# Optimization experiments

Hardware: AMD Instinct MI355X
Metric: run time of the kernel (lower is better)

The kernel has to match this reference:

```python
import jax, jax.numpy as jnp
import numpy as np

N_NODES, N_EDGES, BATCH = 50000, 100000, 256
H = 64            # dim_hidden_features
D_NODE, D_EDGE, D_RBF = 110, 8, 8
D_SET = 2 * H     # Set2Set input_dim = 128, output_dim = 256
D_HID = 512
D_CAT = 54
MP_STEPS, S2S_ITERS = 4, 3


def setup_inputs() -> dict:
    key = jax.random.key(0)
    ks = iter(jax.random.split(key, 48))

    def nrm(shape, s=0.05):
        return jax.random.normal(next(ks), shape, dtype=jnp.float32) * s

    inp = {}
    inp["node_attribute"] = jax.random.normal(next(ks), (N_NODES, D_NODE), dtype=jnp.float32)
    inp["edge_attribute"] = jax.random.normal(next(ks), (N_EDGES, D_EDGE), dtype=jnp.float32)
    inp["edge_length"] = jax.random.uniform(next(ks), (N_EDGES,), dtype=jnp.float32)
    inp["src"] = jax.random.randint(next(ks), (N_EDGES,), 0, N_NODES, dtype=jnp.int32)
    inp["dst"] = jax.random.randint(next(ks), (N_EDGES,), 0, N_NODES, dtype=jnp.int32)
    inp["node_graph"] = jnp.sort(jax.random.randint(next(ks), (N_NODES,), 0, BATCH, dtype=jnp.int32))
    # atom_feature_projector
    inp["proj_W"] = nrm((D_NODE, H)); inp["proj_b"] = jnp.zeros((H,), jnp.float32)
    # RBF layer: centers ~ U(0,1), beta = 10 (per reset_parameters)
    inp["centers"] = jax.random.uniform(next(ks), (D_RBF,), dtype=jnp.float32)
    inp["beta"] = jnp.full((D_RBF,), 10.0, jnp.float32)
    # NNConv edge function: Linear(16 -> 64*64), plus NNConv bias
    inp["bond_W"] = nrm((D_EDGE + D_RBF, H * H)); inp["bond_b"] = jnp.zeros((H * H,), jnp.float32)
    inp["conv_b"] = jnp.zeros((H,), jnp.float32)
    # GRU (input H, hidden H); PyTorch layout (3H, in)
    inp["gru_Wih"] = nrm((3 * H, H)); inp["gru_Whh"] = nrm((3 * H, H))
    inp["gru_bih"] = jnp.zeros((3 * H,), jnp.float32); inp["gru_bhh"] = jnp.zeros((3 * H,), jnp.float32)
    # Set2Set LSTM: input 2*D_SET=256, hidden D_SET=128, 2 layers; PyTorch layout (4H, in)
    inp["lstm_Wih0"] = nrm((4 * D_SET, 2 * D_SET)); inp["lstm_Whh0"] = nrm((4 * D_SET, D_SET))
    inp["lstm_bih0"] = jnp.zeros((4 * D_SET,), jnp.float32); inp["lstm_bhh0"] = jnp.zeros((4 * D_SET,), jnp.float32)
    inp["lstm_Wih1"] = nrm((4 * D_SET, D_SET)); inp["lstm_Whh1"] = nrm((4 * D_SET, D_SET))
    inp["lstm_bih1"] = jnp.zeros((4 * D_SET,), jnp.float32); inp["lstm_bhh1"] = jnp.zeros((4 * D_SET,), jnp.float32)
    # sparsify: Linear(256 -> 512) + PReLU(init 0.25)
    inp["sp_W"] = nrm((2 * D_SET, D_HID)); inp["sp_b"] = jnp.zeros((D_HID,), jnp.float32)
    inp["prelu_a"] = jnp.array([0.25], jnp.float32)
    # catalyst1 head: hiddens[0] (512->512 ReLU, 512->512 Tanh) then outputs[0] (512->54)
    inp["h0_W1"] = nrm((D_HID, D_HID)); inp["h0_b1"] = jnp.zeros((D_HID,), jnp.float32)
    inp["h0_W2"] = nrm((D_HID, D_HID)); inp["h0_b2"] = jnp.zeros((D_HID,), jnp.float32)
    inp["out_W"] = nrm((D_HID, D_CAT)); inp["out_b"] = jnp.zeros((D_CAT,), jnp.float32)
    return inp


def _lstm_cell(x, h, c, Wih, Whh, bih, bhh):
    # PyTorch LSTM gate order: i, f, g, o
    g = x @ Wih.T + bih + h @ Whh.T + bhh
    i, f, gg, o = jnp.split(g, 4, axis=-1)
    c = jax.nn.sigmoid(f) * c + jax.nn.sigmoid(i) * jnp.tanh(gg)
    h = jax.nn.sigmoid(o) * jnp.tanh(c)
    return h, c


def reference(node_attribute, edge_attribute, edge_length, src, dst, node_graph,
              proj_W, proj_b, centers, beta, bond_W, bond_b, conv_b,
              gru_Wih, gru_Whh, gru_bih, gru_bhh,
              lstm_Wih0, lstm_Whh0, lstm_bih0, lstm_bhh0,
              lstm_Wih1, lstm_Whh1, lstm_bih1, lstm_bhh1,
              sp_W, sp_b, prelu_a, h0_W1, h0_b1, h0_W2, h0_b2, out_W, out_b):
    n_nodes = node_attribute.shape[0]
    # atom feature projection
    x = jax.nn.relu(node_attribute @ proj_W + proj_b)                       # (N, H)
    # edge features = [edge_attribute, RBF(length)]
    rbf = jnp.exp(-beta * (edge_length[:, None] - centers[None, :]) ** 2)   # (E, 8)
    efeat = jnp.concatenate([edge_attribute, rbf], axis=-1)                 # (E, 16)
    # NNConv per-edge weight matrix; edge features are constant over MP steps
    W_e = (efeat @ bond_W + bond_b).reshape(-1, H, H)                       # (E, H, H)

    feat, h = x, x
    for _ in range(MP_STEPS):
        # NNConv: message = h_src @ W_e, sum-aggregated at dst, plus bias
        m = jnp.einsum('ei,eio->eo', feat[src], W_e)                        # (E, H)
        agg = jax.ops.segment_sum(m, dst, num_segments=n_nodes) + conv_b    # (N, H)
        gx = jax.nn.relu(agg)
        # GRU cell (PyTorch gate order r, z, n)
        gi = gx @ gru_Wih.T + gru_bih
        gh = h @ gru_Whh.T + gru_bhh
        i_r, i_z, i_n = jnp.split(gi, 3, axis=-1)
        h_r, h_z, h_n = jnp.split(gh, 3, axis=-1)
        r = jax.nn.sigmoid(i_r + h_r)
        z = jax.nn.sigmoid(i_z + h_z)
        n = jnp.tanh(i_n + r * h_n)
        h = (1.0 - z) * n + z * h
        feat = h
    node_agg = jnp.concatenate([feat, x], axis=-1)                          # (N, 2H)

    # Set2Set pooling over graphs (segment softmax attention, 2-layer LSTM)
    B = BATCH
    h0 = c0 = jnp.zeros((B, D_SET), node_agg.dtype)
    h1 = c1 = jnp.zeros((B, D_SET), node_agg.dtype)
    q_star = jnp.zeros((B, 2 * D_SET), node_agg.dtype)
    for _ in range(S2S_ITERS):
        h0, c0 = _lstm_cell(q_star, h0, c0, lstm_Wih0, lstm_Whh0, lstm_bih0, lstm_bhh0)
        h1, c1 = _lstm_cell(h0, h1, c1, lstm_Wih1, lstm_Whh1, lstm_bih1, lstm_bhh1)
        q = h1                                                              # (B, 128)
        e = jnp.sum(node_agg * q[node_graph], axis=-1)                      # (N,)
        emax = jax.ops.segment_max(e, node_graph, num_segments=B)
        p = jnp.exp(e - emax[node_graph])
        denom = jax.ops.segment_sum(p, node_graph, num_segments=B)
        alpha = p / denom[node_graph]                                       # per-graph softmax
        r_out = jax.ops.segment_sum(node_agg * alpha[:, None], node_graph, num_segments=B)
        q_star = jnp.concatenate([q, r_out], axis=-1)                       # (B, 256)

    # sparsify (Linear + PReLU)
    feats = q_star @ sp_W + sp_b                                            # (B, 512)
    feats = jnp.where(feats >= 0, feats, prelu_a * feats)
    # catalyst1 head
    hid = jnp.tanh(jax.nn.relu(feats @ h0_W1 + h0_b1) @ h0_W2 + h0_b2)
    return jax.nn.softmax(hid @ out_W + out_b, axis=-1)                     # (B, 54)
```

## Files before the change

kernel.cpp:

```cpp
#include <hip/hip_runtime.h>
#include <math.h>

constexpr int N = 50000;
constexpr int E = 100000;
constexpr int B = 256;
constexpr int H = 64;
constexpr int DN = 110;
constexpr int NBLK = (E + 63) / 64;

#define DEV __device__ __forceinline__

typedef __attribute__((ext_vector_type(8))) short short8;
typedef __attribute__((ext_vector_type(4))) float floatx4;

DEV float sigf(float x) { return 1.0f / (1.0f + expf(-x)); }

DEV short f2bf(float f) {
    unsigned u = __float_as_uint(f);
    unsigned r = (u + 0x7fffu + ((u >> 16) & 1u)) >> 16;
    return (short)r;
}
DEV float bf2f(short s) { return __uint_as_float(((unsigned)(unsigned short)s) << 16); }

DEV void cvt8(const float* p, short8& hi, short8& lo) {
    float4 u0 = *(const float4*)p;
    float4 u1 = *(const float4*)(p + 4);
    float vv[8] = {u0.x, u0.y, u0.z, u0.w, u1.x, u1.y, u1.z, u1.w};
#pragma unroll
    for (int j = 0; j < 8; ++j) {
        short hb = f2bf(vv[j]);
        hi[j] = hb;
        lo[j] = f2bf(vv[j] - bf2f(hb));
    }
}

__global__ void k_izero(int* p, int n) {
    int i = blockIdx.x * 256 + threadIdx.x;
    if (i < n) p[i] = 0;
}

DEV void d_transpose(const float* in, float* out, int R, int C, int idx) {
    int r = idx / C, c = idx % C;
    out[c * R + r] = in[idx];
}

DEV void d_prepB(const float* __restrict__ W, short* __restrict__ out,
                 int NT16, int ld, int trans, int ocap, int kcap, int idx) {
    int lane = idx & 63;
    int t = idx >> 6;
    int ntile = t % NT16;
    int kt = t / NT16;
    int quad = lane >> 4, col = lane & 15;
    int o = ntile * 16 + col;
    short hi[8], lo[8];
#pragma unroll
    for (int j = 0; j < 8; ++j) {
        int k = kt * 32 + quad * 8 + j;
        float v = 0.0f;
        if (o < ocap && k < kcap) v = trans ? W[(size_t)o * ld + k] : W[(size_t)k * ld + o];
        short hb = f2bf(v);
        hi[j] = hb;
        lo[j] = f2bf(v - bf2f(hb));
    }
    short* dh = out + (((size_t)(t * 2 + 0) * 64 + lane) * 8);
    short* dl = out + (((size_t)(t * 2 + 1) * 64 + lane) * 8);
#pragma unroll
    for (int j = 0; j < 8; ++j) { dh[j] = hi[j]; dl[j] = lo[j]; }
}

DEV void d_prepW(const float* __restrict__ bond_W, const float* __restrict__ bond_b,
                 short* __restrict__ wf, int idx) {
    int lane = idx & 63;
    int t = idx >> 6;
    int ks = t & 1;
    int nt = (t >> 1) & 3;
    int kk = t >> 3;
    const float* S = (kk < 16) ? (bond_W + kk * 4096) : bond_b;
    int quad = lane >> 4, col = lane & 15;
    short hi[8], lo[8];
#pragma unroll
    for (int j = 0; j < 8; ++j) {
        int i = ks * 32 + quad * 8 + j;
        float v = S[i * 64 + nt * 16 + col];
        short hb = f2bf(v);
        hi[j] = hb;
        lo[j] = f2bf(v - bf2f(hb));
    }
    short* dh = wf + (((size_t)(t * 2 + 0) * 64 + lane) * 8);
    short* dl = wf + (((size_t)(t * 2 + 1) * 64 + lane) * 8);
#pragma unroll
    for (int j = 0; j < 8; ++j) { dh[j] = hi[j]; dl[j] = lo[j]; }
}

__launch_bounds__(256)
__global__ void k_prep0(const float* lWih0, const float* lWhh0, const float* lWih1, const float* lWhh1,
                        float* lW0T, float* lU0T, float* lW1T, float* lU1T,
                        const float* bond_W, const float* bond_b, short* wf,
                        const float* gru_Wih, const float* gru_Whh, short* fgI, short* fgH,
                        const float* proj_W, short* fproj,
                        float* zreg) {
    int idx = blockIdx.x * 256 + threadIdx.x;
    if (idx < 131072) { d_transpose(lWih0, lW0T, 512, 256, idx); return; }
    idx -= 131072;
    if (idx < 65536) { d_transpose(lWhh0, lU0T, 512, 128, idx); return; }
    idx -= 65536;
    if (idx < 65536) { d_transpose(lWih1, lW1T, 512, 128, idx); return; }
    idx -= 65536;
    if (idx < 65536) { d_transpose(lWhh1, lU1T, 512, 128, idx); return; }
    idx -= 65536;
    if (idx < 8704) { d_prepW(bond_W, bond_b, wf, idx); return; }
    idx -= 8704;
    if (idx < 1536) { d_prepB(gru_Wih, fgI, 12, 64, 1, 192, 64, idx); return; }
    idx -= 1536;
    if (idx < 1536) { d_prepB(gru_Whh, fgH, 12, 64, 1, 192, 64, idx); return; }
    idx -= 1536;
    if (idx < 1024) { d_prepB(proj_W, fproj, 4, 64, 0, 64, DN, idx); return; }
    idx -= 1024;
    if (idx < 196608) { zreg[idx] = 0.0f; return; }
}
constexpr int PREP0_TOTAL = 131072 + 3 * 65536 + 8704 + 2 * 1536 + 1024 + 196608;

__launch_bounds__(256)
__global__ void k_prephead(const float* sp_W, short* fsp, const float* h0_W1, short* fw1,
                           const float* h0_W2, short* fw2, const float* out_W, short* fow) {
    int idx = blockIdx.x * 256 + threadIdx.x;
    if (idx < 16384) { d_prepB(sp_W, fsp, 32, 512, 0, 512, 256, idx); return; }
    idx -= 16384;
    if (idx < 32768) { d_prepB(h0_W1, fw1, 32, 512, 0, 512, 512, idx); return; }
    idx -= 32768;
    if (idx < 32768) { d_prepB(h0_W2, fw2, 32, 512, 0, 512, 512, idx); return; }
    idx -= 32768;
    if (idx < 4096) { d_prepB(out_W, fow, 4, 54, 0, 54, 512, idx); return; }
}
constexpr int PREPH_TOTAL = 16384 + 2 * 32768 + 4096;

__global__ void k_deg(const int* __restrict__ dst, int* __restrict__ deg) {
    int e = blockIdx.x * 256 + threadIdx.x;
    if (e < E) atomicAdd(&deg[dst[e]], 1);
}
__global__ void k_scan1(const int* __restrict__ deg, int* __restrict__ bsum) {
    __shared__ int s[256];
    int b = blockIdx.x, tid = threadIdx.x;
    int idx = b * 256 + tid;
    s[tid] = (idx < N) ? deg[idx] : 0;
    __syncthreads();
    for (int st = 128; st > 0; st >>= 1) {
        if (tid < st) s[tid] += s[tid + st];
        __syncthreads();
    }
    if (tid == 0) bsum[b] = s[0];
}
__global__ void k_scan2p(int* __restrict__ bsum, int nb) {
    __shared__ int s[256];
    int tid = threadIdx.x;
    int v = (tid < nb) ? bsum[tid] : 0;
    s[tid] = v;
    __syncthreads();
    for (int off = 1; off < 256; off <<= 1) {
        int t = (tid >= off) ? s[tid - off] : 0;
        __syncthreads();
        s[tid] += t;
        __syncthreads();
    }
    if (tid < nb) bsum[tid] = s[tid] - v;
}
__global__ void k_scan3(const int* __restrict__ deg, const int* __restrict__ bsum,
                        int* __restrict__ cursor, int* __restrict__ roff) {
    __shared__ int s[256];
    int b = blockIdx.x, tid = threadIdx.x;
    int idx = b * 256 + tid;
    int v = (idx < N) ? deg[idx] : 0;
    s[tid] = v;
    __syncthreads();
    for (int off = 1; off < 256; off <<= 1) {
        int t = (tid >= off) ? s[tid - off] : 0;
        __syncthreads();
        s[tid] += t;
        __syncthreads();
    }
    if (idx < N) {
        int start = bsum[b] + s[tid] - v;
        cursor[idx] = start;
        roff[idx] = start;
    }
    if (idx == 0) roff[N] = E;
}
__global__ void k_scat(const int* __restrict__ src, const int* __restrict__ dst,
                       int* __restrict__ cursor, int* __restrict__ srcp,
                       int* __restrict__ epos, int* __restrict__ dstp) {
    int e = blockIdx.x * 256 + threadIdx.x;
    if (e >= E) return;
    int d = dst[e];
    int pos = atomicAdd(&cursor[d], 1);
    srcp[pos] = src[e];
    dstp[pos] = d;
    epos[e] = pos;
}

__launch_bounds__(256)
__global__ void k_projm(const float* __restrict__ na, const short* __restrict__ fp,
                        const float* __restrict__ b, float* __restrict__ x,
                        short* __restrict__ hs) {
    __shared__ float as[16 * 132];
    int tid = threadIdx.x, lane = tid & 63, nt = tid >> 6;
    int quad = lane >> 4, col = lane & 15;
    int s0 = blockIdx.x * 16;
    for (int i = tid; i < 16 * DN; i += 256) {
        int r = i / DN, c = i % DN;
        as[r * 132 + c] = na[(size_t)s0 * DN + i];
    }
    for (int i = tid; i < 16 * 22; i += 256) {
        int r = i / 22, c = DN + i % 22;
        as[r * 132 + c] = 0.0f;
    }
    __syncthreads();
    const short8* F = (const short8*)fp;
    floatx4 T = {0.0f, 0.0f, 0.0f, 0.0f};
#pragma unroll
    for (int kt = 0; kt < 4; ++kt) {
        const float* ap = as + col * 132 + kt * 32 + quad * 8;
        short8 ah, al;
#pragma unroll
        for (int j = 0; j < 8; ++j) {
            float v = ap[j];
            short hb = f2bf(v);
            ah[j] = hb;
            al[j] = f2bf(v - bf2f(hb));
        }
        int t = kt * 4 + nt;
        short8 bh = F[(t * 2 + 0) * 64 + lane];
        short8 bl = F[(t * 2 + 1) * 64 + lane];
        T = __builtin_amdgcn_mfma_f32_16x16x32_bf16(ah, bh, T, 0, 0, 0);
        T = __builtin_amdgcn_mfma_f32_16x16x32_bf16(al, bh, T, 0, 0, 0);
        T = __builtin_amdgcn_mfma_f32_16x16x32_bf16(ah, bl, T, 0, 0, 0);
    }
    int o = nt * 16 + col;
    float bo = b[o];
#pragma unroll
    for (int r = 0; r < 4; ++r) {
        int n = s0 + quad * 4 + r;
        float v = fmaxf(T[r] + bo, 0.0f);
        x[(size_t)n * 64 + o] = v;
        short hb = f2bf(v);
        hs[(size_t)n * 128 + o] = hb;
        hs[(size_t)n * 128 + 64 + o] = f2bf(v - bf2f(hb));
    }
}

__global__ void k_efeat2(const float* __restrict__ ea, const float* __restrict__ el,
                         const float* __restrict__ centers, const float* __restrict__ beta,
                         const int* __restrict__ epos, float* __restrict__ ef_t) {
    int e = blockIdx.x * 256 + threadIdx.x;
    if (e >= E) return;
    int pos = epos[e];
    float L = el[e];
#pragma unroll
    for (int j = 0; j < 8; ++j) ef_t[j * E + pos] = ea[e * 8 + j];
#pragma unroll
    for (int j = 0; j < 8; ++j) {
        float d = L - centers[j];
        ef_t[(8 + j) * E + pos] = expf(-beta[j] * d * d);
    }
    ef_t[16 * E + pos] = 1.0f;
}

__launch_bounds__(256)
__global__ void k_msgagg(const short* __restrict__ hs, const float* __restrict__ ef_t,
                         const short* __restrict__ wf, const int* __restrict__ srcp,
                         const int* __restrict__ dstp,
                         float* __restrict__ agg, float* __restrict__ bpart) {
    __shared__ float efs[17 * 64];
    __shared__ int srcs[64];
    __shared__ int dsh[64];
    __shared__ int shprev;
    __shared__ float Csh[64][68];
    __shared__ float psum[4][64], ssum[4][64];
    __shared__ int pd[4], sd[4], whole[4];

    int tid = threadIdx.x;
    int e0 = blockIdx.x * 64;
    int lane = tid & 63;
    int nt = tid >> 6;
    int quad = lane >> 4, col = lane & 15;

    if (tid < 64) {
        int eg = e0 + tid;
        srcs[tid] = (eg < E) ? srcp[eg] : 0;
        dsh[tid] = (eg < E) ? dstp[eg] : N;
    }
    if (tid == 0) shprev = (e0 == 0) ? -1 : dstp[e0 - 1];
    for (int i = tid; i < 17 * 64; i += 256) {
        int kk = i >> 6, e = i & 63;
        int eg = e0 + e;
        efs[i] = (eg < E) ? ef_t[(size_t)kk * E + eg] : 0.0f;
    }
    __syncthreads();

    short8 Ah[4][2], Al[4][2];
#pragma unroll
    for (int mt = 0; mt < 4; ++mt) {
        int s = srcs[mt * 16 + col];
        const short* hp = hs + (size_t)s * 128 + quad * 8;
#pragma unroll
        for (int ks = 0; ks < 2; ++ks) {
            Ah[mt][ks] = *(const short8*)(hp + ks * 32);
            Al[mt][ks] = *(const short8*)(hp + 64 + ks * 32);
        }
    }

    const short8* Wf = (const short8*)wf;
    float C[4][4] = {};

#define LOADB(d0, d1, d2, d3, KK)                      \
    {                                                  \
        int tb_ = ((KK) * 4 + nt) * 2;                 \
        d0 = Wf[((tb_ + 0) * 2 + 0) * 64 + lane];      \
        d1 = Wf[((tb_ + 1) * 2 + 0) * 64 + lane];      \
        d2 = Wf[((tb_ + 0) * 2 + 1) * 64 + lane];      \
        d3 = Wf[((tb_ + 1) * 2 + 1) * 64 + lane];      \
    }

    short8 c0, c1, c2, c3, n0_, n1_, n2_, n3_, q0, q1, q2, q3;
    LOADB(c0, c1, c2, c3, 0);
    LOADB(n0_, n1_, n2_, n3_, 1);
    LOADB(q0, q1, q2, q3, 2);

#pragma unroll 1
    for (int kk = 0; kk < 17; ++kk) {
        int kn = kk + 3;
        if (kn > 16) kn = 16;
        short8 p0, p1, p2, p3;
        LOADB(p0, p1, p2, p3, kn);

#pragma unroll
        for (int mt = 0; mt < 4; ++mt) {
            floatx4 T = {0.0f, 0.0f, 0.0f, 0.0f};
            T = __builtin_amdgcn_mfma_f32_16x16x32_bf16(Ah[mt][0], c0, T, 0, 0, 0);
            T = __builtin_amdgcn_mfma_f32_16x16x32_bf16(Ah[mt][1], c1, T, 0, 0, 0);
            T = __builtin_amdgcn_mfma_f32_16x16x32_bf16(Al[mt][0], c0, T, 0, 0, 0);
            T = __builtin_amdgcn_mfma_f32_16x16x32_bf16(Al[mt][1], c1, T, 0, 0, 0);
            T = __builtin_amdgcn_mfma_f32_16x16x32_bf16(Ah[mt][0], c2, T, 0, 0, 0);
            T = __builtin_amdgcn_mfma_f32_16x16x32_bf16(Ah[mt][1], c3, T, 0, 0, 0);
            float4 ef = *(const float4*)&efs[kk * 64 + mt * 16 + quad * 4];
            C[mt][0] += ef.x * T[0];
            C[mt][1] += ef.y * T[1];
            C[mt][2] += ef.z * T[2];
            C[mt][3] += ef.w * T[3];
        }
        c0 = n0_; c1 = n1_; c2 = n2_; c3 = n3_;
        n0_ = q0; n1_ = q1; n2_ = q2; n3_ = q3;
        q0 = p0; q1 = p1; q2 = p2; q3 = p3;
    }
#undef LOADB

#pragma unroll
    for (int mt = 0; mt < 4; ++mt)
#pragma unroll
        for (int r = 0; r < 4; ++r)
            Csh[mt * 16 + quad * 4 + r][nt * 16 + col] = C[mt][r];
    __syncthreads();

    {
        int c = lane;
        int base = nt * 16;
        int prevd = (nt == 0) ? shprev : dsh[base - 1];
        int cur = dsh[base];
        int gcap = cur < N ? cur : N;
        for (int q = prevd + 1; q < gcap; ++q) agg[(size_t)q * 64 + c] = 0.0f;
        if (cur >= N) {
            if (lane == 0) { pd[nt] = -2; sd[nt] = -2; whole[nt] = 0; }
        } else {
            float acc = 0.0f;
            int ntr = 0;
            bool done = false;
            for (int r = base; r < base + 16; ++r) {
                int d = dsh[r];
                if (d != cur) {
                    if (ntr == 0) {
                        psum[nt][c] = acc;
                        if (lane == 0) pd[nt] = cur;
                    } else {
                        agg[(size_t)cur * 64 + c] = acc;
                    }
                    ++ntr;
                    int dc = d < N ? d : N;
                    for (int q = cur + 1; q < dc; ++q) agg[(size_t)q * 64 + c] = 0.0f;
                    cur = d; acc = 0.0f;
                    if (cur >= N) { done = true; break; }
                }
                acc += Csh[r][c];
            }
            if (!done) {
                if (ntr == 0) {
                    psum[nt][c] = acc;
                    if (lane == 0) { pd[nt] = cur; sd[nt] = cur; whole[nt] = 1; }
                } else {
                    ssum[nt][c] = acc;
                    if (lane == 0) { sd[nt] = cur; whole[nt] = 0; }
                }
            } else {
                if (lane == 0) { sd[nt] = -2; whole[nt] = 0; }
            }
        }
    }
    __syncthreads();

    if (tid < 64) {
        int c = tid;
        int cur = -1;
        float acc = 0.0f;
        bool ownedCur = false;
        bool first = true;
        int firstd = dsh[0];
#pragma unroll
        for (int w = 0; w < 4; ++w) {
            int p = pd[w];
            if (p < 0) continue;
            float s = psum[w][c];
            if (first) {
                cur = p; acc = s;
                ownedCur = (e0 == 0) || (firstd != shprev);
                first = false;
            } else if (p == cur) {
                acc += s;
            } else {
                if (ownedCur) agg[(size_t)cur * 64 + c] = acc;
                else bpart[(size_t)blockIdx.x * 64 + c] = acc;
                cur = p; acc = s; ownedCur = true;
            }
            if (!whole[w] && sd[w] >= 0) {
                int sdd = sd[w];
                float s2 = ssum[w][c];
                if (sdd == cur) {
                    acc += s2;
                } else {
                    if (ownedCur) agg[(size_t)cur * 64 + c] = acc;
                    else bpart[(size_t)blockIdx.x * 64 + c] = acc;
                    cur = sdd; acc = s2; ownedCur = true;
                }
            }
        }
        if (!first) {
            if (ownedCur) agg[(size_t)cur * 64 + c] = acc;
            else bpart[(size_t)blockIdx.x * 64 + c] = acc;
        }
    }
}

__launch_bounds__(256)
__global__ void k_gru4(const float* __restrict__ agg, const float* __restrict__ bpart,
                       const int* __restrict__ roff, const float* __restrict__ conv_b,
                       short* __restrict__ hs,
                       const short* __restrict__ fI, const short* __restrict__ fH,
                       const float* __restrict__ bih, const float* __restrict__ bhh) {
    int tid = threadIdx.x, lane = tid & 63, nt = tid >> 6;
    int quad = lane >> 4, col = lane & 15;
    int n0 = blockIdx.x * 32;

    short8 Gh[2][2], Gl[2][2], Hh[2][2], Hl[2][2];
#pragma unroll
    for (int mt = 0; mt < 2; ++mt) {
        int node = n0 + mt * 16 + col;
        bool ok = node < N;
        int nc = ok ? node : (N - 1);
        float acc[2][8];
        const float* ag = agg + (size_t)nc * 64;
#pragma unroll
        for (int ks = 0; ks < 2; ++ks) {
            const float* cb = conv_b + ks * 32 + quad * 8;
            float4 a0 = *(const float4*)(ag + ks * 32 + quad * 8);
            float4 a1 = *(const float4*)(ag + ks * 32 + quad * 8 + 4);
            acc[ks][0] = a0.x + cb[0]; acc[ks][1] = a0.y + cb[1];
            acc[ks][2] = a0.z + cb[2]; acc[ks][3] = a0.w + cb[3];
            acc[ks][4] = a1.x + cb[4]; acc[ks][5] = a1.y + cb[5];
            acc[ks][6] = a1.z + cb[6]; acc[ks][7] = a1.w + cb[7];
        }
        int rs = roff[nc];
        int re = roff[nc + 1];
        if (re > rs) {
            int b0 = rs >> 6, b1 = (re - 1) >> 6;
            for (int bb = b0 + 1; bb <= b1; ++bb) {
                const float* bp = bpart + (size_t)bb * 64;
#pragma unroll
                for (int ks = 0; ks < 2; ++ks) {
                    float4 p0 = *(const float4*)(bp + ks * 32 + quad * 8);
                    float4 p1 = *(const float4*)(bp + ks * 32 + quad * 8 + 4);
                    acc[ks][0] += p0.x; acc[ks][1] += p0.y;
                    acc[ks][2] += p0.z; acc[ks][3] += p0.w;
                    acc[ks][4] += p1.x; acc[ks][5] += p1.y;
                    acc[ks][6] += p1.z; acc[ks][7] += p1.w;
                }
            }
        }
        const short* hp = hs + (size_t)nc * 128 + quad * 8;
#pragma unroll
        for (int ks = 0; ks < 2; ++ks) {
            short8 hh8 = *(const short8*)(hp + ks * 32);
            short8 hl8 = *(const short8*)(hp + 64 + ks * 32);
            Hh[mt][ks] = hh8;
            Hl[mt][ks] = hl8;
#pragma unroll
            for (int j = 0; j < 8; ++j) {
                float g = ok ? fmaxf(acc[ks][j], 0.0f) : 0.0f;
                short gb = f2bf(g);
                Gh[mt][ks][j] = gb;
                Gl[mt][ks][j] = f2bf(g - bf2f(gb));
            }
        }
        if (!ok) {
#pragma unroll
            for (int ks = 0; ks < 2; ++ks) {
                Hh[mt][ks] = short8{0,0,0,0,0,0,0,0};
                Hl[mt][ks] = short8{0,0,0,0,0,0,0,0};
            }
        }
    }
    __syncthreads();

    const short8* FI = (const short8*)fI;
    const short8* FH = (const short8*)fH;
    floatx4 aI[2][3] = {}, aH[2][3] = {};
#pragma unroll
    for (int ks = 0; ks < 2; ++ks) {
        short8 bIh[3], bIl[3], bHh[3], bHl[3];
#pragma unroll
        for (int g = 0; g < 3; ++g) {
            int t = ks * 12 + g * 4 + nt;
            bIh[g] = FI[(t * 2 + 0) * 64 + lane];
            bIl[g] = FI[(t * 2 + 1) * 64 + lane];
            bHh[g] = FH[(t * 2 + 0) * 64 + lane];
            bHl[g] = FH[(t * 2 + 1) * 64 + lane];
        }
#pragma unroll
        for (int mt = 0; mt < 2; ++mt) {
#pragma unroll
            for (int g = 0; g < 3; ++g) {
                aI[mt][g] = __builtin_amdgcn_mfma_f32_16x16x32_bf16(Gh[mt][ks], bIh[g], aI[mt][g], 0, 0, 0);
                aI[mt][g] = __builtin_amdgcn_mfma_f32_16x16x32_bf16(Gl[mt][ks], bIh[g], aI[mt][g], 0, 0, 0);
                aI[mt][g] = __builtin_amdgcn_mfma_f32_16x16x32_bf16(Gh[mt][ks], bIl[g], aI[mt][g], 0, 0, 0);
                aH[mt][g] = __builtin_amdgcn_mfma_f32_16x16x32_bf16(Hh[mt][ks], bHh[g], aH[mt][g], 0, 0, 0);
                aH[mt][g] = __builtin_amdgcn_mfma_f32_16x16x32_bf16(Hl[mt][ks], bHh[g], aH[mt][g], 0, 0, 0);
                aH[mt][g] = __builtin_amdgcn_mfma_f32_16x16x32_bf16(Hh[mt][ks], bHl[g], aH[mt][g], 0, 0, 0);
            }
        }
    }

    int o = nt * 16 + col;
    float br = bih[o], bz = bih[64 + o], bn = bih[128 + o];
    float cr = bhh[o], cz = bhh[64 + o], cn = bhh[128 + o];
#pragma unroll
    for (int mt = 0; mt < 2; ++mt) {
#pragma unroll
        for (int r = 0; r < 4; ++r) {
            int node = n0 + mt * 16 + quad * 4 + r;
            if (node >= N) continue;
            float rg = sigf(aI[mt][0][r] + br + aH[mt][0][r] + cr);
            float z  = sigf(aI[mt][1][r] + bz + aH[mt][1][r] + cz);
            float ng = tanhf(aI[mt][2][r] + bn + rg * (aH[mt][2][r] + cn));
            size_t hb_ = (size_t)node * 128 + o;
            float hold = bf2f(hs[hb_]) + bf2f(hs[hb_ + 64]);
            float hn = (1.0f - z) * ng + z * hold;
            short hi = f2bf(hn);
            hs[hb_] = hi;
            hs[hb_ + 64] = f2bf(hn - bf2f(hi));
        }
    }
}

__global__ void k_bounds2(const int* __restrict__ ng, int* __restrict__ gs, int* __restrict__ ge) {
    int n = blockIdx.x * 256 + threadIdx.x;
    if (n >= N) return;
    int g = ng[n];
    int gp = (n == 0) ? -1 : ng[n - 1];
    if (g != gp) {
        gs[g] = n;
        if (n > 0) ge[gp] = n;
        for (int q = gp + 1; q < g; ++q) { gs[q] = 0; ge[q] = 0; }
    }
    if (n == N - 1) {
        ge[g] = N;
        for (int q = g + 1; q < B; ++q) { gs[q] = 0; ge[q] = 0; }
    }
}

__launch_bounds__(256)
__global__ void k_s2s(float* __restrict__ h0, float* __restrict__ c0,
                      float* __restrict__ h1, float* __restrict__ c1,
                      float* __restrict__ q_star,
                      const float* __restrict__ W0T, const float* __restrict__ U0T,
                      const float* __restrict__ b0i, const float* __restrict__ b0h,
                      const float* __restrict__ W1T, const float* __restrict__ U1T,
                      const float* __restrict__ b1i, const float* __restrict__ b1h,
                      const short* __restrict__ hs, const float* __restrict__ x,
                      const int* __restrict__ gs, const int* __restrict__ ge) {
    __shared__ float xb[256], hb[128], gb[512], h0n[128], qv[128];
    __shared__ float mrg[4][2][64];
    __shared__ float ml[4][2];
    int g = blockIdx.x, tid = threadIdx.x;
    xb[tid] = q_star[g * 256 + tid];
    if (tid < 128) hb[tid] = h0[g * 128 + tid];
    __syncthreads();
    float g0 = b0i[tid] + b0h[tid];
    float g1 = b0i[tid + 256] + b0h[tid + 256];
    for (int i = 0; i < 256; ++i) {
        float xx = xb[i];
        g0 += xx * W0T[i * 512 + tid];
        g1 += xx * W0T[i * 512 + tid + 256];
    }
    for (int i = 0; i < 128; ++i) {
        float hh = hb[i];
        g0 += hh * U0T[i * 512 + tid];
        g1 += hh * U0T[i * 512 + tid + 256];
    }
    gb[tid] = g0; gb[tid + 256] = g1;
    __syncthreads();
    if (tid < 128) {
        float ii = gb[tid], ff = gb[128 + tid], gg = gb[256 + tid], oo = gb[384 + tid];
        float c = sigf(ff) * c0[g * 128 + tid] + sigf(ii) * tanhf(gg);
        float hn = sigf(oo) * tanhf(c);
        c0[g * 128 + tid] = c; h0[g * 128 + tid] = hn; h0n[tid] = hn;
        hb[tid] = h1[g * 128 + tid];
    }
    __syncthreads();
    float ga = b1i[tid] + b1h[tid];
    float gbv = b1i[tid + 256] + b1h[tid + 256];
    for (int i = 0; i < 128; ++i) {
        float xx = h0n[i], hh = hb[i];
        ga  += xx * W1T[i * 512 + tid]       + hh * U1T[i * 512 + tid];
        gbv += xx * W1T[i * 512 + tid + 256] + hh * U1T[i * 512 + tid + 256];
    }
    gb[tid] = ga; gb[tid + 256] = gbv;
    __syncthreads();
    if (tid < 128) {
        float ii = gb[tid], ff = gb[128 + tid], gg = gb[256 + tid], oo = gb[384 + tid];
        float c = sigf(ff) * c1[g * 128 + tid] + sigf(ii) * tanhf(gg);
        float hn = sigf(oo) * tanhf(c);
        c1[g * 128 + tid] = c; h1[g * 128 + tid] = hn;
        q_star[g * 256 + tid] = hn;
        qv[tid] = hn;
    }
    __syncthreads();
    int s0v = gs[g], s1v = ge[g];
    int lane = tid & 63, grp = tid >> 6;
    float qh = qv[lane], qx = qv[64 + lane];
    float mM = -INFINITY, lL = 0.0f, nh = 0.0f, nx = 0.0f;
    for (int n = s0v + grp; n < s1v; n += 16) {
        float hv[4], xv[4], e[4];
#pragma unroll
        for (int j = 0; j < 4; ++j) {
            int nj = n + 4 * j;
            int nc = (nj < s1v) ? nj : n;
            hv[j] = bf2f(hs[(size_t)nc * 128 + lane]) + bf2f(hs[(size_t)nc * 128 + 64 + lane]);
            xv[j] = x[(size_t)nc * 64 + lane];
            e[j] = hv[j] * qh + xv[j] * qx;
        }
#pragma unroll
        for (int off = 32; off; off >>= 1) {
#pragma unroll
            for (int j = 0; j < 4; ++j) e[j] += __shfl_xor(e[j], off, 64);
        }
#pragma unroll
        for (int j = 0; j < 4; ++j)
            if (n + 4 * j >= s1v) e[j] = -INFINITY;
        float mb = fmaxf(fmaxf(e[0], e[1]), fmaxf(e[2], e[3]));
        float mn = fmaxf(mM, mb);
        float sc = expf(mM - mn);
        float w0 = expf(e[0] - mn), w1 = expf(e[1] - mn);
        float w2 = expf(e[2] - mn), w3 = expf(e[3] - mn);
        lL = lL * sc + ((w0 + w1) + (w2 + w3));
        nh = nh * sc + ((w0 * hv[0] + w1 * hv[1]) + (w2 * hv[2] + w3 * hv[3]));
        nx = nx * sc + ((w0 * xv[0] + w1 * xv[1]) + (w2 * xv[2] + w3 * xv[3]));
        mM = mn;
    }
    mrg[grp][0][lane] = nh;
    mrg[grp][1][lane] = nx;
    if (lane == 0) { ml[grp][0] = mM; ml[grp][1] = lL; }
    __syncthreads();
    if (tid < 128) {
        int half = tid >> 6, dl = tid & 63;
        float M = -INFINITY;
#pragma unroll
        for (int i = 0; i < 4; ++i) M = fmaxf(M, ml[i][0]);
        float L = 0.0f, NUM = 0.0f;
#pragma unroll
        for (int i = 0; i < 4; ++i) {
            float sc = expf(ml[i][0] - M);
            L += ml[i][1] * sc;
            NUM += mrg[i][half][dl] * sc;
        }
        q_star[g * 256 + 128 + tid] = (s1v > s0v) ? NUM / L : 0.0f;
    }
}

template<int MODE>
__launch_bounds__(256)
__global__ void k_hgemm(const float* __restrict__ A, const short* __restrict__ Bf,
                        const float* __restrict__ bias, const float* __restrict__ pa,
                        float* __restrict__ Cout, int K, int NT16) {
    int tid = threadIdx.x, lane = tid & 63, nt = tid >> 6;
    int quad = lane >> 4, col = lane & 15;
    int s0 = blockIdx.x * 16;
    int ntile = blockIdx.y * 4 + nt;
    int NoutTot = NT16 * 16;
    const short8* F = (const short8*)Bf;
    floatx4 T = {0.0f, 0.0f, 0.0f, 0.0f};
    const float* ap = A + (size_t)(s0 + col) * K + quad * 8;
    int KT = K >> 5;
#pragma unroll 4
    for (int kt = 0; kt < KT; ++kt) {
        short8 ah, al;
        cvt8(ap + kt * 32, ah, al);
        int t = kt * NT16 + ntile;
        short8 bh = F[(t * 2 + 0) * 64 + lane];
        short8 bl = F[(t * 2 + 1) * 64 + lane];
        T = __builtin_amdgcn_mfma_f32_16x16x32_bf16(ah, bh, T, 0, 0, 0);
        T = __builtin_amdgcn_mfma_f32_16x16x32_bf16(al, bh, T, 0, 0, 0);
        T = __builtin_amdgcn_mfma_f32_16x16x32_bf16(ah, bl, T, 0, 0, 0);
    }
    int o = ntile * 16 + col;
    float b = bias[o];
    float a = (MODE == 0) ? pa[0] : 0.0f;
#pragma unroll
    for (int r = 0; r < 4; ++r) {
        float v = T[r] + b;
        if (MODE == 0) v = (v >= 0.0f) ? v : a * v;
        if (MODE == 1) v = fmaxf(v, 0.0f);
        if (MODE == 2) v = tanhf(v);
        Cout[(size_t)(s0 + quad * 4 + r) * NoutTot + o] = v;
    }
}

__launch_bounds__(256)
__global__ void k_hout(const float* __restrict__ A, const short* __restrict__ Bf,
                       const float* __restrict__ ob, float* __restrict__ out) {
    __shared__ float sm[16][64];
    __shared__ float smax[16], sinv[16];
    int tid = threadIdx.x, lane = tid & 63, nt = tid >> 6;
    int quad = lane >> 4, col = lane & 15;
    int s0 = blockIdx.x * 16;
    const short8* F = (const short8*)Bf;
    floatx4 T = {0.0f, 0.0f, 0.0f, 0.0f};
    const float* ap = A + (size_t)(s0 + col) * 512 + quad * 8;
#pragma unroll 4
    for (int kt = 0; kt < 16; ++kt) {
        short8 ah, al;
        cvt8(ap + kt * 32, ah, al);
        int t = kt * 4 + nt;
        short8 bh = F[(t * 2 + 0) * 64 + lane];
        short8 bl = F[(t * 2 + 1) * 64 + lane];
        T = __builtin_amdgcn_mfma_f32_16x16x32_bf16(ah, bh, T, 0, 0, 0);
        T = __builtin_amdgcn_mfma_f32_16x16x32_bf16(al, bh, T, 0, 0, 0);
        T = __builtin_amdgcn_mfma_f32_16x16x32_bf16(ah, bl, T, 0, 0, 0);
    }
    int o = nt * 16 + col;
    float b = (o < 54) ? ob[o] : 0.0f;
#pragma unroll
    for (int r = 0; r < 4; ++r)
        sm[quad * 4 + r][o] = (o < 54) ? (T[r] + b) : -1e30f;
    __syncthreads();
    if (tid < 16) {
        float m = -INFINITY;
        for (int j = 0; j < 54; ++j) m = fmaxf(m, sm[tid][j]);
        float s = 0.0f;
        for (int j = 0; j < 54; ++j) s += expf(sm[tid][j] - m);
        smax[tid] = m;
        sinv[tid] = 1.0f / s;
    }
    __syncthreads();
    for (int idx = tid; idx < 16 * 54; idx += 256) {
        int srow = idx / 54, oo = idx % 54;
        out[(size_t)(s0 + srow) * 54 + oo] = expf(sm[srow][oo] - smax[srow]) * sinv[srow];
    }
}

extern "C" void kernel_launch(void* const* d_in, const int* in_sizes, int n_in,
                              void* d_out, int out_size, void* d_ws, size_t ws_size,
                              hipStream_t stream) {
    const float* node_attr = (const float*)d_in[0];
    const float* edge_attr = (const float*)d_in[1];
    const float* edge_len  = (const float*)d_in[2];
    const int*   src       = (const int*)d_in[3];
    const int*   dst       = (const int*)d_in[4];
    const int*   node_grph = (const int*)d_in[5];
    const float* proj_W    = (const float*)d_in[6];
    const float* proj_b    = (const float*)d_in[7];
    const float* centers   = (const float*)d_in[8];
    const float* beta      = (const float*)d_in[9];
    const float* bond_W    = (const float*)d_in[10];
    const float* bond_b    = (const float*)d_in[11];
    const float* conv_b    = (const float*)d_in[12];
    const float* gru_Wih   = (const float*)d_in[13];
    const float* gru_Whh   = (const float*)d_in[14];
    const float* gru_bih   = (const float*)d_in[15];
    const float* gru_bhh   = (const float*)d_in[16];
    const float* lWih0     = (const float*)d_in[17];
    const float* lWhh0     = (const float*)d_in[18];
    const float* lbih0     = (const float*)d_in[19];
    const float* lbhh0     = (const float*)d_in[20];
    const float* lWih1     = (const float*)d_in[21];
    const float* lWhh1     = (const float*)d_in[22];
    const float* lbih1     = (const float*)d_in[23];
    const float* lbhh1     = (const float*)d_in[24];
    const float* sp_W      = (const float*)d_in[25];
    const float* sp_b      = (const float*)d_in[26];
    const float* prelu_a   = (const float*)d_in[27];
    const float* h0_W1     = (const float*)d_in[28];
    const float* h0_b1     = (const float*)d_in[29];
    const float* h0_W2     = (const float*)d_in[30];
    const float* h0_b2     = (const float*)d_in[31];
    const float* out_W     = (const float*)d_in[32];
    const float* out_b     = (const float*)d_in[33];
    float* out = (float*)d_out;

    float* ws = (float*)d_ws;
    size_t off = 0;
    float* x      = ws + off; off += (size_t)N * 64;
    float* hsf    = ws + off; off += (size_t)N * 64;
    float* ef_t   = ws + off; off += (size_t)E * 17;
    float* agg    = ws + off; off += (size_t)N * 64;
    float* wfrag  = ws + off; off += 17 * 16 * 64 * 8 / 2;
    float* fgI    = ws + off; off += 2 * 64 * 192 / 2;
    float* fgH    = ws + off; off += 2 * 64 * 192 / 2;
    float* fproj  = ws + off; off += 16 * 1024 / 2;
    float* lW0T   = ws + off; off += 256 * 512;
    float* lU0T   = ws + off; off += 128 * 512;
    float* lW1T   = ws + off; off += 128 * 512;
    float* lU1T   = ws + off; off += 128 * 512;
    float* h0     = ws + off; off += B * 128;
    float* c0     = ws + off; off += B * 128;
    float* h1     = ws + off; off += B * 128;
    float* c1     = ws + off; off += B * 128;
    float* q_star = ws + off; off += B * 256;
    float* bpart  = ws + off; off += (size_t)NBLK * 64;
    int* gs       = (int*)(ws + off); off += B;
    int* ge       = (int*)(ws + off); off += B;
    int* deg      = (int*)(ws + off); off += N;
    int* cursor   = (int*)(ws + off); off += N;
    int* roff     = (int*)(ws + off); off += N + 1;
    int* bsum     = (int*)(ws + off); off += 256;
    int* srcp     = (int*)(ws + off); off += E;
    int* epos     = (int*)(ws + off); off += E;
    int* dstp     = (int*)(ws + off); off += E;

    short* hs = (short*)hsf;

    short* fsp = (short*)ef_t;
    short* fw1 = (short*)(ef_t + 131072);
    short* fw2 = (short*)(ef_t + 131072 + 262144);
    short* fow = (short*)(ef_t + 131072 + 2 * 262144);
    float* hb1 = ef_t + 131072 + 2 * 262144 + 32768;
    float* hb2 = hb1 + 131072;

    constexpr int NB = (N + 255) / 256;

    k_izero<<<NB, 256, 0, stream>>>(deg, N);
    k_deg<<<(E + 255) / 256, 256, 0, stream>>>(dst, deg);
    k_scan1<<<NB, 256, 0, stream>>>(deg, bsum);
    k_scan2p<<<1, 256, 0, stream>>>(bsum, NB);
    k_scan3<<<NB, 256, 0, stream>>>(deg, bsum, cursor, roff);
    k_scat<<<(E + 255) / 256, 256, 0, stream>>>(src, dst, cursor, srcp, epos, dstp);

    k_prep0<<<(PREP0_TOTAL + 255) / 256, 256, 0, stream>>>(
        lWih0, lWhh0, lWih1, lWhh1, lW0T, lU0T, lW1T, lU1T,
        bond_W, bond_b, (short*)wfrag, gru_Wih, gru_Whh, (short*)fgI, (short*)fgH,
        proj_W, (short*)fproj, h0);

    k_projm<<<N / 16, 256, 0, stream>>>(node_attr, (const short*)fproj, proj_b, x, hs);
    k_efeat2<<<(E + 255) / 256, 256, 0, stream>>>(edge_attr, edge_len, centers, beta, epos, ef_t);

    k_bounds2<<<(N + 255) / 256, 256, 0, stream>>>(node_grph, gs, ge);

    for (int step = 0; step < 4; ++step) {
        k_msgagg<<<NBLK, 256, 0, stream>>>(hs, ef_t, (const short*)wfrag, srcp, dstp,
                                           agg, bpart);
        k_gru4<<<(N + 31) / 32, 256, 0, stream>>>(agg, bpart, roff, conv_b, hs,
                                                  (const short*)fgI, (const short*)fgH,
                                                  gru_bih, gru_bhh);
    }

    k_prephead<<<(PREPH_TOTAL + 255) / 256, 256, 0, stream>>>(
        sp_W, fsp, h0_W1, fw1, h0_W2, fw2, out_W, fow);

    for (int it = 0; it < 3; ++it) {
        k_s2s<<<B, 256, 0, stream>>>(h0, c0, h1, c1, q_star,
                                     lW0T, lU0T, lbih0, lbhh0,
                                     lW1T, lU1T, lbih1, lbhh1,
                                     hs, x, gs, ge);
    }

    k_hgemm<0><<<dim3(16, 8), 256, 0, stream>>>(q_star, fsp, sp_b, prelu_a, hb1, 256, 32);
    k_hgemm<1><<<dim3(16, 8), 256, 0, stream>>>(hb1, fw1, h0_b1, nullptr, hb2, 512, 32);
    k_hgemm<2><<<dim3(16, 8), 256, 0, stream>>>(hb2, fw2, h0_b2, nullptr, hb1, 512, 32);
    k_hout<<<16, 256, 0, stream>>>(hb1, fow, out_b, out);
}
```

Measured before the change: 733.4 us.

## Process 128 edges per block in NNConv message kernel to reuse edge weights

Doubles the edges handled per block in the fused message/aggregate kernel from 64 to 128. Each wave now holds eight 16-edge A tiles, so every loaded slice of the edge-network weights feeds twice as many MFMAs. Source-feature gathers are issued straight from global memory ahead of the shared-memory staging to overlap latency. The weight prefetch depth drops from three stages to two to make room in registers. The trade-off is higher register and LDS use, hence lower occupancy, plus half as many blocks and longer serial segment scans.

```diff
diff --git a/kernel.cpp b/kernel.cpp
--- a/kernel.cpp
+++ b/kernel.cpp
@@ -6,7 +6,8 @@
 constexpr int B = 256;
 constexpr int H = 64;
 constexpr int DN = 110;
-constexpr int NBLK = (E + 63) / 64;
+constexpr int EPB = 128;
+constexpr int NBLK = (E + EPB - 1) / EPB;
 
 #define DEV __device__ __forceinline__
 
@@ -269,37 +270,24 @@
                          const short* __restrict__ wf, const int* __restrict__ srcp,
                          const int* __restrict__ dstp,
                          float* __restrict__ agg, float* __restrict__ bpart) {
-    __shared__ float efs[17 * 64];
-    __shared__ int srcs[64];
-    __shared__ int dsh[64];
+    __shared__ float efs[17 * EPB];
+    __shared__ int dsh[EPB];
     __shared__ int shprev;
-    __shared__ float Csh[64][68];
+    __shared__ float Csh[EPB][68];
     __shared__ float psum[4][64], ssum[4][64];
     __shared__ int pd[4], sd[4], whole[4];
 
     int tid = threadIdx.x;
-    int e0 = blockIdx.x * 64;
+    int e0 = blockIdx.x * EPB;
     int lane = tid & 63;
     int nt = tid >> 6;
     int quad = lane >> 4, col = lane & 15;
 
-    if (tid < 64) {
-        int eg = e0 + tid;
-        srcs[tid] = (eg < E) ? srcp[eg] : 0;
-        dsh[tid] = (eg < E) ? dstp[eg] : N;
-    }
-    if (tid == 0) shprev = (e0 == 0) ? -1 : dstp[e0 - 1];
-    for (int i = tid; i < 17 * 64; i += 256) {
-        int kk = i >> 6, e = i & 63;
-        int eg = e0 + e;
-        efs[i] = (eg < E) ? ef_t[(size_t)kk * E + eg] : 0.0f;
-    }
-    __syncthreads();
-
-    short8 Ah[4][2], Al[4][2];
-#pragma unroll
-    for (int mt = 0; mt < 4; ++mt) {
-        int s = srcs[mt * 16 + col];
+    short8 Ah[8][2], Al[8][2];
+#pragma unroll
+    for (int mt = 0; mt < 8; ++mt) {
+        int eg = e0 + mt * 16 + col;
+        int s = (eg < E) ? srcp[eg] : 0;
         const short* hp = hs + (size_t)s * 128 + quad * 8;
 #pragma unroll
         for (int ks = 0; ks < 2; ++ks) {
@@ -308,8 +296,20 @@
         }
     }
 
+    if (tid < EPB) {
+        int eg = e0 + tid;
+        dsh[tid] = (eg < E) ? dstp[eg] : N;
+    }
+    if (tid == 0) shprev = (e0 == 0) ? -1 : dstp[e0 - 1];
+    for (int i = tid; i < 17 * EPB; i += 256) {
+        int kk = i >> 7, e = i & (EPB - 1);
+        int eg = e0 + e;
+        efs[i] = (eg < E) ? ef_t[(size_t)kk * E + eg] : 0.0f;
+    }
+    __syncthreads();
+
     const short8* Wf = (const short8*)wf;
-    float C[4][4] = {};
+    float C[8][4] = {};
 
 #define LOADB(d0, d1, d2, d3, KK)                      \
     {                                                  \
@@ -320,20 +320,19 @@
         d3 = Wf[((tb_ + 1) * 2 + 1) * 64 + lane];      \
     }
 
-    short8 c0, c1, c2, c3, n0_, n1_, n2_, n3_, q0, q1, q2, q3;
+    short8 c0, c1, c2, c3, n0_, n1_, n2_, n3_;
     LOADB(c0, c1, c2, c3, 0);
     LOADB(n0_, n1_, n2_, n3_, 1);
-    LOADB(q0, q1, q2, q3, 2);
 
 #pragma unroll 1
     for (int kk = 0; kk < 17; ++kk) {
-        int kn = kk + 3;
+        int kn = kk + 2;
         if (kn > 16) kn = 16;
         short8 p0, p1, p2, p3;
         LOADB(p0, p1, p2, p3, kn);
 
 #pragma unroll
-        for (int mt = 0; mt < 4; ++mt) {
+        for (int mt = 0; mt < 8; ++mt) {
             floatx4 T = {0.0f, 0.0f, 0.0f, 0.0f};
             T = __builtin_amdgcn_mfma_f32_16x16x32_bf16(Ah[mt][0], c0, T, 0, 0, 0);
             T = __builtin_amdgcn_mfma_f32_16x16x32_bf16(Ah[mt][1], c1, T, 0, 0, 0);
@@ -341,20 +340,19 @@
             T = __builtin_amdgcn_mfma_f32_16x16x32_bf16(Al[mt][1], c1, T, 0, 0, 0);
             T = __builtin_amdgcn_mfma_f32_16x16x32_bf16(Ah[mt][0], c2, T, 0, 0, 0);
             T = __builtin_amdgcn_mfma_f32_16x16x32_bf16(Ah[mt][1], c3, T, 0, 0, 0);
-            float4 ef = *(const float4*)&efs[kk * 64 + mt * 16 + quad * 4];
+            float4 ef = *(const float4*)&efs[kk * EPB + mt * 16 + quad * 4];
             C[mt][0] += ef.x * T[0];
             C[mt][1] += ef.y * T[1];
             C[mt][2] += ef.z * T[2];
             C[mt][3] += ef.w * T[3];
         }
         c0 = n0_; c1 = n1_; c2 = n2_; c3 = n3_;
-        n0_ = q0; n1_ = q1; n2_ = q2; n3_ = q3;
-        q0 = p0; q1 = p1; q2 = p2; q3 = p3;
+        n0_ = p0; n1_ = p1; n2_ = p2; n3_ = p3;
     }
 #undef LOADB
 
 #pragma unroll
-    for (int mt = 0; mt < 4; ++mt)
+    for (int mt = 0; mt < 8; ++mt)
 #pragma unroll
         for (int r = 0; r < 4; ++r)
             Csh[mt * 16 + quad * 4 + r][nt * 16 + col] = C[mt][r];
@@ -362,7 +360,7 @@
 
     {
         int c = lane;
-        int base = nt * 16;
+        int base = nt * 32;
         int prevd = (nt == 0) ? shprev : dsh[base - 1];
         int cur = dsh[base];
         int gcap = cur < N ? cur : N;
@@ -373,7 +371,7 @@
             float acc = 0.0f;
             int ntr = 0;
             bool done = false;
-            for (int r = base; r < base + 16; ++r) {
+            for (int r = base; r < base + 32; ++r) {
                 int d = dsh[r];
                 if (d != cur) {
                     if (ntr == 0) {
@@ -478,7 +476,7 @@
         int rs = roff[nc];
         int re = roff[nc + 1];
         if (re > rs) {
-            int b0 = rs >> 6, b1 = (re - 1) >> 6;
+            int b0 = rs >> 7, b1 = (re - 1) >> 7;
             for (int bb = b0 + 1; bb <= b1; ++bb) {
                 const float* bp = bpart + (size_t)bb * 64;
 #pragma unroll
```

Result: slower. 784.3 us (+6.9%).
